# Kernel tuning notes

Measured on AMD Instinct MI355X. Metric: run time of the kernel, lower is better.

## Reference

```python
import jax, jax.numpy as jnp
import numpy as np

B = 131072
D = 64
NUM_REL = 32


def setup_inputs() -> dict:
    key = jax.random.key(0)
    k1, k2, k3, k4 = jax.random.split(key, 4)
    embeds1 = jax.random.normal(k1, (B, D), dtype=jnp.float32)
    embeds2 = jax.random.normal(k2, (B, D), dtype=jnp.float32)
    rels = jax.random.randint(k3, (B,), 0, NUM_REL, dtype=jnp.int32)
    # learned relation table: one D*D matrix per relation type
    rel_embeds = jax.random.normal(k4, (NUM_REL, D * D), dtype=jnp.float32)
    return {"embeds1": embeds1, "embeds2": embeds2, "rels": rels,
            "rel_embeds": rel_embeds}


def reference(embeds1, embeds2, rels, rel_embeds):
    # gather per-sample relation matrices: [B, D, D]
    rel_mats = rel_embeds[rels].reshape(-1, D, D)
    # per-sample bilinear form: score_b = e1_b^T R_b e2_b  -> [B]
    e1R = jnp.einsum("bd,bde->be", embeds1, rel_mats)
    return (e1R * embeds2).sum(axis=1)
```

## Files before the change

kernel.cpp:

```cpp
#include <hip/hip_runtime.h>
#include <hip/hip_bf16.h>
#include <cstddef>

#define BB 131072
#define DD 64
#define NREL 32
#define PADN 131584
#define NBLK (PADN / 64)

#define BLOCKS_AC 512
#define SPB (BB / BLOCKS_AC)
#define CHUNKS 8
#define BPC (BLOCKS_AC / CHUNKS)

typedef __attribute__((ext_vector_type(8))) __bf16 bf16x8;
typedef __attribute__((ext_vector_type(4))) float f32x4;

__global__ __launch_bounds__(256) void phaseA_hist(
    const int* __restrict__ rels, int* __restrict__ blockCnt,
    const float* __restrict__ relE, __bf16* __restrict__ Rpre) {
  __shared__ int hist[NREL];
  const int t = threadIdx.x;
  if (t < NREL) hist[t] = 0;
  __syncthreads();
  atomicAdd(&hist[rels[blockIdx.x * 256 + t]], 1);
  __syncthreads();
  if (t < NREL) blockCnt[blockIdx.x * NREL + t] = hist[t];

  if (blockIdx.x < NREL) {
    const int r = blockIdx.x;
    const float* __restrict__ R = relE + (size_t)r * (DD * DD);
    __bf16* __restrict__ dst = Rpre + (size_t)r * 8192;
#pragma unroll
    for (int i = 0; i < 16; ++i) {
      const int idx = i * 256 + t;
      const int g = idx >> 9;
      const int lane = (idx >> 3) & 63;
      const int j = idx & 7;
      const int k = (g >> 2) * 32 + (lane >> 4) * 8 + j;
      const int n = (g & 3) * 16 + (lane & 15);
      const float x = R[k * DD + n];
      const __bf16 hb = (__bf16)x;
      dst[idx] = hb;
      dst[4096 + idx] = (__bf16)(x - (float)hb);
    }
  }
}

__global__ __launch_bounds__(256) void phaseB_scan(
    const int* __restrict__ blockCnt, int* __restrict__ blockOff,
    int* __restrict__ binBase, int* __restrict__ permPacked) {
  __shared__ int partial[CHUNKS][NREL];
  __shared__ int chunkBase[CHUNKS][NREL];
  __shared__ int binB[NREL];
  __shared__ int totS[NREL];
  __shared__ int totalPad;
  const int t = threadIdx.x;
  const int c = t >> 5;
  const int r = t & 31;
  const int b0 = c * BPC;
  int run = 0;
#pragma unroll 4
  for (int b = 0; b < BPC; ++b) run += blockCnt[(b0 + b) * NREL + r];
  partial[c][r] = run;
  __syncthreads();
  if (t < NREL) {
    int acc = 0;
#pragma unroll
    for (int i = 0; i < CHUNKS; ++i) { chunkBase[i][t] = acc; acc += partial[i][t]; }
    totS[t] = acc;
  }
  __syncthreads();
  if (t == 0) {
    int acc = 0;
#pragma unroll
    for (int i = 0; i < NREL; ++i) {
      binB[i] = acc;
      acc += (totS[i] + 15) & ~15;
    }
    totalPad = acc;
  }
  __syncthreads();
  if (t < NREL) {
    binBase[t] = binB[t];
    const int start = binB[t] + totS[t];
    const int end = binB[t] + ((totS[t] + 15) & ~15);
    for (int p = start; p < end; ++p) permPacked[p] = -1;
  }
  for (int p = totalPad + t; p < PADN; p += 256) permPacked[p] = -1;
  int run2 = chunkBase[c][r];
#pragma unroll 4
  for (int b = 0; b < BPC; ++b) {
    blockOff[(b0 + b) * NREL + r] = run2;
    run2 += blockCnt[(b0 + b) * NREL + r];
  }
}

__global__ __launch_bounds__(256) void phaseC_scatter(
    const int* __restrict__ rels, const int* __restrict__ blockOff,
    const int* __restrict__ binBase, int* __restrict__ permPacked) {
  __shared__ int cnt[NREL];
  __shared__ int baseArr[NREL];
  const int t = threadIdx.x;
  if (t < NREL) {
    cnt[t] = 0;
    baseArr[t] = binBase[t] + blockOff[blockIdx.x * NREL + t];
  }
  __syncthreads();
  const int s = blockIdx.x * SPB + t;
  const int rv = rels[s];
  const int rank = atomicAdd(&cnt[rv], 1);
  permPacked[baseArr[rv] + rank] = (rv << 17) | s;
}

__global__ __launch_bounds__(256, 4) void bilinear_mfma16(
    const float* __restrict__ e1g, const float* __restrict__ e2g,
    const __bf16* __restrict__ Rpre, const int* __restrict__ permPacked,
    float* __restrict__ out) {
  const int lane = threadIdx.x & 63;
  const int wv = threadIdx.x >> 6;
  const int l15 = lane & 15;
  const int h2 = lane >> 4;
  const int pk = permPacked[blockIdx.x * 64 + wv * 16 + l15];
  const unsigned long long vm = __ballot(pk >= 0);
  if (vm == 0ull) return;
  const int r0 = __builtin_amdgcn_readlane(pk, (int)__builtin_ctzll(vm)) >> 17;

  const int sa = __shfl(pk, l15) & 0x1FFFF;
  const float4* __restrict__ arow = (const float4*)(e1g + (size_t)sa * DD);

  float e2v[4][4];
#pragma unroll
  for (int reg = 0; reg < 4; ++reg) {
    const int si = __shfl(pk, h2 * 4 + reg) & 0x1FFFF;
    const float* __restrict__ er = e2g + (size_t)si * DD + l15;
#pragma unroll
    for (int nt = 0; nt < 4; ++nt) e2v[reg][nt] = er[nt * 16];
  }

  const bf16x8* __restrict__ bp = (const bf16x8*)(Rpre + (size_t)r0 * 8192);

  f32x4 acc[4];
#pragma unroll
  for (int nt = 0; nt < 4; ++nt)
#pragma unroll
    for (int i = 0; i < 4; ++i) acc[nt][i] = 0.f;

#pragma unroll
  for (int kc = 0; kc < 2; ++kc) {
    const float4 v0 = arow[kc * 8 + h2 * 2];
    const float4 v1 = arow[kc * 8 + h2 * 2 + 1];
    const float x[8] = {v0.x, v0.y, v0.z, v0.w, v1.x, v1.y, v1.z, v1.w};
    bf16x8 aH, aL;
#pragma unroll
    for (int j = 0; j < 8; ++j) {
      const __bf16 hb = (__bf16)x[j];
      aH[j] = hb;
      aL[j] = (__bf16)(x[j] - (float)hb);
    }
#pragma unroll
    for (int nt = 0; nt < 4; ++nt) {
      const int g = kc * 4 + nt;
      const bf16x8 bH = bp[g * 64 + lane];
      const bf16x8 bL = bp[512 + g * 64 + lane];
      acc[nt] = __builtin_amdgcn_mfma_f32_16x16x32_bf16(aH, bH, acc[nt], 0, 0, 0);
      acc[nt] = __builtin_amdgcn_mfma_f32_16x16x32_bf16(aH, bL, acc[nt], 0, 0, 0);
      acc[nt] = __builtin_amdgcn_mfma_f32_16x16x32_bf16(aL, bH, acc[nt], 0, 0, 0);
    }
  }

  float rp[4] = {0.f, 0.f, 0.f, 0.f};
#pragma unroll
  for (int reg = 0; reg < 4; ++reg)
#pragma unroll
    for (int nt = 0; nt < 4; ++nt)
      rp[reg] = fmaf(acc[nt][reg], e2v[reg][nt], rp[reg]);
#pragma unroll
  for (int m = 1; m < 16; m <<= 1)
#pragma unroll
    for (int reg = 0; reg < 4; ++reg) rp[reg] += __shfl_xor(rp[reg], m);
#pragma unroll
  for (int reg = 0; reg < 4; ++reg) {
    const int pkw = __shfl(pk, h2 * 4 + reg);
    if (l15 == reg && pkw >= 0) out[pkw & 0x1FFFF] = rp[reg];
  }
}

extern "C" void kernel_launch(void* const* d_in, const int* in_sizes, int n_in,
                              void* d_out, int out_size, void* d_ws, size_t ws_size,
                              hipStream_t stream) {
  const float* e1 = (const float*)d_in[0];
  const float* e2 = (const float*)d_in[1];
  const int* rels = (const int*)d_in[2];
  const float* relE = (const float*)d_in[3];
  float* out = (float*)d_out;

  int* permPacked = (int*)d_ws;
  int* blockCnt = permPacked + PADN;
  int* blockOff = blockCnt + BLOCKS_AC * NREL;
  int* binBase = blockOff + BLOCKS_AC * NREL;
  __bf16* Rpre = (__bf16*)((char*)d_ws + (1 << 20));

  phaseA_hist<<<BLOCKS_AC, 256, 0, stream>>>(rels, blockCnt, relE, Rpre);
  phaseB_scan<<<1, 256, 0, stream>>>(blockCnt, blockOff, binBase, permPacked);
  phaseC_scatter<<<BLOCKS_AC, 256, 0, stream>>>(rels, blockOff, binBase, permPacked);
  bilinear_mfma16<<<NBLK, 256, 0, stream>>>(e1, e2, Rpre, permPacked, out);
}
```

Before: 117.2 us.

## Drop split-bf16 correction MFMAs and simplify relation bucketing with global atomics

```diff
diff --git a/kernel.cpp b/kernel.cpp
--- a/kernel.cpp
+++ b/kernel.cpp
@@ -5,140 +5,110 @@
 #define BB 131072
 #define DD 64
 #define NREL 32
-#define PADN 131584
-#define NBLK (PADN / 64)
+#define MAXW 8224
+#define NBLK (MAXW / 4)
 
-#define BLOCKS_AC 512
-#define SPB (BB / BLOCKS_AC)
-#define CHUNKS 8
-#define BPC (BLOCKS_AC / CHUNKS)
+#define BLOCKS_S 256
+#define SPS (BB / BLOCKS_S)
 
 typedef __attribute__((ext_vector_type(8))) __bf16 bf16x8;
 typedef __attribute__((ext_vector_type(4))) float f32x4;
 
-__global__ __launch_bounds__(256) void phaseA_hist(
-    const int* __restrict__ rels, int* __restrict__ blockCnt,
-    const float* __restrict__ relE, __bf16* __restrict__ Rpre) {
-  __shared__ int hist[NREL];
+__global__ __launch_bounds__(256) void sort_scatter(
+    const int* __restrict__ rels, int* __restrict__ binCnt,
+    int* __restrict__ perm, const float* __restrict__ relE,
+    __bf16* __restrict__ Rpre) {
+  __shared__ int hist[NREL], baseS[NREL], cnt[NREL];
   const int t = threadIdx.x;
-  if (t < NREL) hist[t] = 0;
+  if (t < NREL) { hist[t] = 0; cnt[t] = 0; }
   __syncthreads();
-  atomicAdd(&hist[rels[blockIdx.x * 256 + t]], 1);
+  const int s0 = blockIdx.x * SPS + t;
+  const int rv0 = rels[s0];
+  const int rv1 = rels[s0 + 256];
+  atomicAdd(&hist[rv0], 1);
+  atomicAdd(&hist[rv1], 1);
   __syncthreads();
-  if (t < NREL) blockCnt[blockIdx.x * NREL + t] = hist[t];
-
+  if (t < NREL) baseS[t] = atomicAdd(&binCnt[t], hist[t]);
+  __syncthreads();
+  {
+    const int rank = atomicAdd(&cnt[rv0], 1);
+    perm[(size_t)rv0 * BB + baseS[rv0] + rank] = s0;
+  }
+  {
+    const int rank = atomicAdd(&cnt[rv1], 1);
+    perm[(size_t)rv1 * BB + baseS[rv1] + rank] = s0 + 256;
+  }
   if (blockIdx.x < NREL) {
     const int r = blockIdx.x;
     const float* __restrict__ R = relE + (size_t)r * (DD * DD);
-    __bf16* __restrict__ dst = Rpre + (size_t)r * 8192;
+    __bf16* __restrict__ dst = Rpre + (size_t)r * 4096;
 #pragma unroll
     for (int i = 0; i < 16; ++i) {
       const int idx = i * 256 + t;
       const int g = idx >> 9;
-      const int lane = (idx >> 3) & 63;
+      const int ln = (idx >> 3) & 63;
       const int j = idx & 7;
-      const int k = (g >> 2) * 32 + (lane >> 4) * 8 + j;
-      const int n = (g & 3) * 16 + (lane & 15);
-      const float x = R[k * DD + n];
-      const __bf16 hb = (__bf16)x;
-      dst[idx] = hb;
-      dst[4096 + idx] = (__bf16)(x - (float)hb);
+      const int k = (g >> 2) * 32 + (ln >> 4) * 8 + j;
+      const int n = (g & 3) * 16 + (ln & 15);
+      dst[idx] = (__bf16)R[k * DD + n];
     }
   }
 }
 
-__global__ __launch_bounds__(256) void phaseB_scan(
-    const int* __restrict__ blockCnt, int* __restrict__ blockOff,
-    int* __restrict__ binBase, int* __restrict__ permPacked) {
-  __shared__ int partial[CHUNKS][NREL];
-  __shared__ int chunkBase[CHUNKS][NREL];
-  __shared__ int binB[NREL];
-  __shared__ int totS[NREL];
-  __shared__ int totalPad;
+__global__ __launch_bounds__(256) void tiny_scan(
+    const int* __restrict__ binCnt, unsigned* __restrict__ waveTbl) {
+  __shared__ int wStart[NREL + 1];
   const int t = threadIdx.x;
-  const int c = t >> 5;
-  const int r = t & 31;
-  const int b0 = c * BPC;
-  int run = 0;
-#pragma unroll 4
-  for (int b = 0; b < BPC; ++b) run += blockCnt[(b0 + b) * NREL + r];
-  partial[c][r] = run;
-  __syncthreads();
-  if (t < NREL) {
-    int acc = 0;
-#pragma unroll
-    for (int i = 0; i < CHUNKS; ++i) { chunkBase[i][t] = acc; acc += partial[i][t]; }
-    totS[t] = acc;
-  }
-  __syncthreads();
   if (t == 0) {
     int acc = 0;
 #pragma unroll
-    for (int i = 0; i < NREL; ++i) {
-      binB[i] = acc;
-      acc += (totS[i] + 15) & ~15;
+    for (int r = 0; r < NREL; ++r) {
+      wStart[r] = acc;
+      acc += (binCnt[r] + 15) >> 4;
     }
-    totalPad = acc;
+    wStart[NREL] = acc;
   }
   __syncthreads();
-  if (t < NREL) {
-    binBase[t] = binB[t];
-    const int start = binB[t] + totS[t];
-    const int end = binB[t] + ((totS[t] + 15) & ~15);
-    for (int p = start; p < end; ++p) permPacked[p] = -1;
-  }
-  for (int p = totalPad + t; p < PADN; p += 256) permPacked[p] = -1;
-  int run2 = chunkBase[c][r];
-#pragma unroll 4
-  for (int b = 0; b < BPC; ++b) {
-    blockOff[(b0 + b) * NREL + r] = run2;
-    run2 += blockCnt[(b0 + b) * NREL + r];
-  }
-}
-
-__global__ __launch_bounds__(256) void phaseC_scatter(
-    const int* __restrict__ rels, const int* __restrict__ blockOff,
-    const int* __restrict__ binBase, int* __restrict__ permPacked) {
-  __shared__ int cnt[NREL];
-  __shared__ int baseArr[NREL];
-  const int t = threadIdx.x;
-  if (t < NREL) {
-    cnt[t] = 0;
-    baseArr[t] = binBase[t] + blockOff[blockIdx.x * NREL + t];
-  }
-  __syncthreads();
-  const int s = blockIdx.x * SPB + t;
-  const int rv = rels[s];
-  const int rank = atomicAdd(&cnt[rv], 1);
-  permPacked[baseArr[rv] + rank] = (rv << 17) | s;
+  const int r = t >> 3;
+  const int sub = t & 7;
+  const int w0 = wStart[r];
+  const int w1 = wStart[r + 1];
+  for (int w = w0 + sub; w < w1; w += 8)
+    waveTbl[w] = ((unsigned)r << 20) | (unsigned)((w - w0) * 16);
+  for (int w = wStart[NREL] + t; w < MAXW; w += 256)
+    waveTbl[w] = 0x000FFFFFu;
 }
 
 __global__ __launch_bounds__(256, 4) void bilinear_mfma16(
     const float* __restrict__ e1g, const float* __restrict__ e2g,
-    const __bf16* __restrict__ Rpre, const int* __restrict__ permPacked,
+    const __bf16* __restrict__ Rpre, const int* __restrict__ perm,
+    const unsigned* __restrict__ waveTbl, const int* __restrict__ binCnt,
     float* __restrict__ out) {
   const int lane = threadIdx.x & 63;
   const int wv = threadIdx.x >> 6;
   const int l15 = lane & 15;
   const int h2 = lane >> 4;
-  const int pk = permPacked[blockIdx.x * 64 + wv * 16 + l15];
-  const unsigned long long vm = __ballot(pk >= 0);
-  if (vm == 0ull) return;
-  const int r0 = __builtin_amdgcn_readlane(pk, (int)__builtin_ctzll(vm)) >> 17;
+  const unsigned tbl = waveTbl[blockIdx.x * 4 + wv];
+  const int r = (int)(tbl >> 20);
+  const int off0 = (int)(tbl & 0xFFFFF);
+  const int nv0 = binCnt[r] - off0;
+  if (nv0 <= 0) return;
+  const int nv = nv0 < 16 ? nv0 : 16;
+  const int sl = l15 < nv ? l15 : nv - 1;
+  const int pk = perm[(size_t)r * BB + off0 + sl];
 
-  const int sa = __shfl(pk, l15) & 0x1FFFF;
-  const float4* __restrict__ arow = (const float4*)(e1g + (size_t)sa * DD);
+  const float4* __restrict__ arow = (const float4*)(e1g + (size_t)pk * DD);
 
   float e2v[4][4];
 #pragma unroll
   for (int reg = 0; reg < 4; ++reg) {
-    const int si = __shfl(pk, h2 * 4 + reg) & 0x1FFFF;
+    const int si = __shfl(pk, h2 * 4 + reg);
     const float* __restrict__ er = e2g + (size_t)si * DD + l15;
 #pragma unroll
     for (int nt = 0; nt < 4; ++nt) e2v[reg][nt] = er[nt * 16];
   }
 
-  const bf16x8* __restrict__ bp = (const bf16x8*)(Rpre + (size_t)r0 * 8192);
+  const bf16x8* __restrict__ bp = (const bf16x8*)(Rpre + (size_t)r * 4096);
 
   f32x4 acc[4];
 #pragma unroll
@@ -151,21 +121,13 @@
     const float4 v0 = arow[kc * 8 + h2 * 2];
     const float4 v1 = arow[kc * 8 + h2 * 2 + 1];
     const float x[8] = {v0.x, v0.y, v0.z, v0.w, v1.x, v1.y, v1.z, v1.w};
-    bf16x8 aH, aL;
+    bf16x8 aH;
 #pragma unroll
-    for (int j = 0; j < 8; ++j) {
-      const __bf16 hb = (__bf16)x[j];
-      aH[j] = hb;
-      aL[j] = (__bf16)(x[j] - (float)hb);
-    }
+    for (int j = 0; j < 8; ++j) aH[j] = (__bf16)x[j];
 #pragma unroll
     for (int nt = 0; nt < 4; ++nt) {
-      const int g = kc * 4 + nt;
-      const bf16x8 bH = bp[g * 64 + lane];
-      const bf16x8 bL = bp[512 + g * 64 + lane];
+      const bf16x8 bH = bp[(kc * 4 + nt) * 64 + lane];
       acc[nt] = __builtin_amdgcn_mfma_f32_16x16x32_bf16(aH, bH, acc[nt], 0, 0, 0);
-      acc[nt] = __builtin_amdgcn_mfma_f32_16x16x32_bf16(aH, bL, acc[nt], 0, 0, 0);
-      acc[nt] = __builtin_amdgcn_mfma_f32_16x16x32_bf16(aL, bH, acc[nt], 0, 0, 0);
     }
   }
 
@@ -182,7 +144,7 @@
 #pragma unroll
   for (int reg = 0; reg < 4; ++reg) {
     const int pkw = __shfl(pk, h2 * 4 + reg);
-    if (l15 == reg && pkw >= 0) out[pkw & 0x1FFFF] = rp[reg];
+    if (l15 == reg && h2 * 4 + reg < nv) out[pkw] = rp[reg];
   }
 }
 
@@ -195,14 +157,13 @@
   const float* relE = (const float*)d_in[3];
   float* out = (float*)d_out;
 
-  int* permPacked = (int*)d_ws;
-  int* blockCnt = permPacked + PADN;
-  int* blockOff = blockCnt + BLOCKS_AC * NREL;
-  int* binBase = blockOff + BLOCKS_AC * NREL;
-  __bf16* Rpre = (__bf16*)((char*)d_ws + (1 << 20));
+  int* perm = (int*)d_ws;
+  int* binCnt = (int*)((char*)d_ws + (16u << 20));
+  unsigned* waveTbl = (unsigned*)((char*)d_ws + (16u << 20) + 128);
+  __bf16* Rpre = (__bf16*)((char*)d_ws + (17u << 20));
 
-  phaseA_hist<<<BLOCKS_AC, 256, 0, stream>>>(rels, blockCnt, relE, Rpre);
-  phaseB_scan<<<1, 256, 0, stream>>>(blockCnt, blockOff, binBase, permPacked);
-  phaseC_scatter<<<BLOCKS_AC, 256, 0, stream>>>(rels, blockOff, binBase, permPacked);
-  bilinear_mfma16<<<NBLK, 256, 0, stream>>>(e1, e2, Rpre, permPacked, out);
+  hipMemsetAsync(binCnt, 0, NREL * sizeof(int), stream);
+  sort_scatter<<<BLOCKS_S, 256, 0, stream>>>(rels, binCnt, perm, relE, Rpre);
+  tiny_scan<<<1, 256, 0, stream>>>(binCnt, waveTbl);
+  bilinear_mfma16<<<NBLK, 256, 0, stream>>>(e1, e2, Rpre, perm, waveTbl, binCnt, out);
 }
```

Result: faster. 114.7 us (-2.2%).
